# Performance work log

Measured on AMD Instinct MI355X. Metric: run time of the kernel, lower is better.

Reference implementation:

```python
import jax, jax.numpy as jnp
import numpy as np

N_NODES = 50000
EPS = 1e-7      # GENConv message epsilon
BN_EPS = 1e-5   # BatchNorm1d eps
N_AGGR = 2


def setup_inputs() -> dict:
    key = jax.random.key(0)
    ks = jax.random.split(key, 8)
    C = 64
    E = 800000
    x = jax.random.normal(ks[0], (N_NODES, C), dtype=jnp.float32)
    edge_index = jax.random.randint(ks[1], (2, E), 0, N_NODES, dtype=jnp.int64)
    # per-GENConv MLP params, stacked over the N_AGGR layers
    W1 = jax.random.normal(ks[2], (N_AGGR, C, 2 * C), dtype=jnp.float32) * (1.0 / np.sqrt(C))
    b1 = jnp.zeros((N_AGGR, 2 * C), dtype=jnp.float32)
    gamma = jnp.ones((N_AGGR, 2 * C), dtype=jnp.float32)
    beta = jnp.zeros((N_AGGR, 2 * C), dtype=jnp.float32)
    W2 = jax.random.normal(ks[3], (N_AGGR, 2 * C, C), dtype=jnp.float32) * (1.0 / np.sqrt(2 * C))
    b2 = jnp.zeros((N_AGGR, C), dtype=jnp.float32)
    t = jnp.ones((N_AGGR,), dtype=jnp.float32)  # learnable softmax temperature
    return {"x": x, "edge_index": edge_index, "W1": W1, "b1": b1,
            "gamma": gamma, "beta": beta, "W2": W2, "b2": b2, "t": t}


def _gen_conv(x, src, dst, W1_l, b1_l, gamma_l, beta_l, W2_l, b2_l, t_l):
    # message: relu(x_j) + eps  (edge_attr is None)
    m = jax.nn.relu(x[src]) + EPS                      # [E, C]
    # softmax aggregation over edges grouped by destination node
    logits = m * t_l                                   # [E, C]
    seg_max = jax.ops.segment_max(logits, dst, num_segments=N_NODES)  # [N, C]
    ex = jnp.exp(logits - seg_max[dst])                # [E, C]
    den = jax.ops.segment_sum(ex, dst, num_segments=N_NODES)          # [N, C]
    alpha = ex / (den[dst] + 1e-16)                    # [E, C]
    aggr = jax.ops.segment_sum(m * alpha, dst, num_segments=N_NODES)  # [N, C]
    # residual then MLP: Linear(C,2C) -> BatchNorm1d (train-mode stats) -> ReLU -> Linear(2C,C)
    h = aggr + x
    h = h @ W1_l + b1_l                                # [N, 2C]
    mean = h.mean(axis=0)
    var = h.var(axis=0)                                # biased variance (torch BN)
    h = (h - mean) / jnp.sqrt(var + BN_EPS) * gamma_l + beta_l
    h = jax.nn.relu(h)
    h = h @ W2_l + b2_l                                # [N, C]
    return h


def reference(x, edge_index, W1, b1, gamma, beta, W2, b2, t):
    src = edge_index[0]
    dst = edge_index[1]
    for l in range(N_AGGR):
        x = _gen_conv(x, src, dst, W1[l], b1[l], gamma[l], beta[l], W2[l], b2[l], t[l])
        x = jax.nn.relu(x)
        # dropout in eval mode == identity
    return x
```

## Files before the change

kernel.cpp:

```cpp
#include <hip/hip_runtime.h>
#include <math.h>

#define NN 50000
#define EPSM 1e-7f
#define BN_EPS 1e-5f
#define NBK 391


__global__ __launch_bounds__(256) void bucket_hist_kernel(
    const int* __restrict__ dst, int* __restrict__ bhist, int E,
    unsigned* __restrict__ mm0, float* __restrict__ bn0){
  __shared__ int h[NBK];
  int t = threadIdx.x;
  if (blockIdx.x == 0){
    if (t < 64) mm0[t] = 0x7F7FFFFFu;
    else if (t < 128) mm0[t] = 0u;
    bn0[t] = 0.f;
  }
  for (int i = t; i < NBK; i += 256) h[i] = 0;
  __syncthreads();
  int e0 = blockIdx.x * 4096;
  int cnt = min(4096, E - e0);
  for (int i = t; i < cnt; i += 256) atomicAdd(&h[dst[e0 + i] >> 7], 1);
  __syncthreads();
  for (int i = t; i < NBK; i += 256) if (h[i]) atomicAdd(&bhist[i], h[i]);
}

__global__ void bucket_scan_kernel(const int* __restrict__ bhist,
                                   int* __restrict__ bbase, int* __restrict__ gcur){
  int lane = threadIdx.x;
  int loc[7]; int s = 0;
#pragma unroll
  for (int k = 0; k < 7; ++k){
    int i = lane * 7 + k;
    int v = (i < NBK) ? bhist[i] : 0;
    loc[k] = s; s += v;
  }
  int sc = s;
#pragma unroll
  for (int o = 1; o < 64; o <<= 1){
    int n = __shfl_up(sc, o);
    if (lane >= o) sc += n;
  }
  int exc = sc - s;
#pragma unroll
  for (int k = 0; k < 7; ++k){
    int i = lane * 7 + k;
    if (i < NBK){ bbase[i] = exc + loc[k]; gcur[i] = exc + loc[k]; }
    else if (i == NBK) bbase[i] = exc + loc[k];
  }
}

__global__ __launch_bounds__(256) void bucket_scatter_kernel(
    const int* __restrict__ src, const int* __restrict__ dst,
    int* __restrict__ gcur, unsigned* __restrict__ packed_g, int E){
  __shared__ int hist[NBK], offs[NBK], gb[NBK], curk[NBK];
  __shared__ unsigned stage[4096];
  __shared__ int gpos[4096];
  int t = threadIdx.x;
  for (int i = t; i < NBK; i += 256) hist[i] = 0;
  __syncthreads();
  int e0 = blockIdx.x * 4096;
  int cnt = min(4096, E - e0);
  unsigned pk[16]; int bk[16];
  int nmine = 0;
  for (int i = t; i < cnt; i += 256){
    int d = dst[e0 + i], s = src[e0 + i];
    pk[nmine] = ((unsigned)d << 16) | (unsigned)s;
    bk[nmine] = d >> 7;
    atomicAdd(&hist[bk[nmine]], 1);
    ++nmine;
  }
  __syncthreads();
  if (t < 64){
    int loc[7]; int s = 0;
#pragma unroll
    for (int k = 0; k < 7; ++k){
      int i = t * 7 + k;
      int v = (i < NBK) ? hist[i] : 0;
      loc[k] = s; s += v;
    }
    int sc = s;
#pragma unroll
    for (int o = 1; o < 64; o <<= 1){
      int n = __shfl_up(sc, o);
      if (t >= o) sc += n;
    }
    int exc = sc - s;
#pragma unroll
    for (int k = 0; k < 7; ++k){
      int i = t * 7 + k;
      if (i < NBK) offs[i] = exc + loc[k];
    }
  }
  __syncthreads();
  for (int i = t; i < NBK; i += 256){
    int h = hist[i];
    gb[i] = h ? atomicAdd(&gcur[i], h) : 0;
    curk[i] = offs[i];
  }
  __syncthreads();
  for (int k = 0; k < nmine; ++k){
    int b = bk[k];
    int p = atomicAdd(&curk[b], 1);
    stage[p] = pk[k];
    gpos[p] = gb[b] + (p - offs[b]);
  }
  __syncthreads();
  for (int j = t; j < cnt; j += 256) packed_g[gpos[j]] = stage[j];
}

__global__ __launch_bounds__(256) void bucket_place_kernel(
    const unsigned* __restrict__ packed_g, const int* __restrict__ bbase,
    int* __restrict__ start_g, int* __restrict__ end_g,
    unsigned short* __restrict__ srcs_g, int N){
  __shared__ int deg[128], off[128], cur[128];
  __shared__ int sstage[4096];
  int b = blockIdx.x, t = threadIdx.x;
  int beg = bbase[b], cnt = bbase[b + 1] - beg;
  if (t < 128) deg[t] = 0;
  __syncthreads();
  for (int j = t; j < cnt; j += 256)
    atomicAdd(&deg[(packed_g[beg + j] >> 16) & 127], 1);
  __syncthreads();
  if (t < 64){
    int i0 = t * 2;
    int v0 = deg[i0], v1 = deg[i0 + 1];
    int s = v0 + v1;
    int sc = s;
#pragma unroll
    for (int o = 1; o < 64; o <<= 1){
      int n = __shfl_up(sc, o);
      if (t >= o) sc += n;
    }
    int exc = sc - s;
    off[i0] = exc; off[i0 + 1] = exc + v0;
  }
  __syncthreads();
  int node0 = b * 128;
  if (t < 128){
    int node = node0 + t;
    if (node < N){
      start_g[node] = beg + off[t];
      end_g[node] = beg + off[t] + deg[t];
    }
    cur[t] = off[t];
  }
  __syncthreads();
  if (cnt <= 4096){
    for (int j = t; j < cnt; j += 256){
      unsigned p = packed_g[beg + j];
      int lp = atomicAdd(&cur[(p >> 16) & 127], 1);
      sstage[lp] = (int)(p & 0xFFFFu);
    }
    __syncthreads();
    for (int j = t; j < cnt; j += 256)
      srcs_g[beg + j] = (unsigned short)sstage[j];
  } else {
    for (int j = t; j < cnt; j += 256){
      unsigned p = packed_g[beg + j];
      int lp = atomicAdd(&cur[(p >> 16) & 127], 1);
      srcs_g[beg + lp] = (unsigned short)(p & 0xFFFFu);
    }
  }
}


__global__ __launch_bounds__(256) void colminmax_kernel(
    const float* __restrict__ x, unsigned* __restrict__ mm,
    unsigned short* __restrict__ mh, int N){
  __shared__ unsigned smn[256], smx[256];
  int c = threadIdx.x & 63;
  int half = c >> 5, cc = c & 31;
  unsigned short* mhh = mh + (size_t)half * N * 32;
  int slot = blockIdx.x * 4 + (threadIdx.x >> 6);
  float mx = 0.f, mn = 1e30f;
  for (int r = slot; r < N; r += 256 * 4){
    float m = fmaxf(x[r * 64 + c], 0.f) + EPSM;
    unsigned u = __float_as_uint(m);
    u += 0x7FFFu + ((u >> 16) & 1u);
    unsigned short us = (unsigned short)(u >> 16);
    mhh[r * 32 + cc] = us;
    float mb = __uint_as_float(((unsigned)us) << 16);
    mx = fmaxf(mx, mb);
    mn = fminf(mn, mb);
  }
  smn[threadIdx.x] = __float_as_uint(mn);
  smx[threadIdx.x] = __float_as_uint(mx);
  __syncthreads();
  if (threadIdx.x < 64){
    unsigned a = smn[c], b = smn[c + 64], d = smn[c + 128], e = smn[c + 192];
    atomicMin(&mm[c], min(min(a, b), min(d, e)));
    a = smx[c]; b = smx[c + 64]; d = smx[c + 128]; e = smx[c + 192];
    atomicMax(&mm[64 + c], max(max(a, b), max(d, e)));
  }
}


__global__ __launch_bounds__(256) void aggregate_kernel(
    const float* __restrict__ x, const unsigned short* __restrict__ mh,
    const int* __restrict__ start, const int* __restrict__ segend,
    const unsigned short* __restrict__ srcs, const float* __restrict__ tptr,
    int layer, const unsigned* __restrict__ mm, float* __restrict__ h0, int N){
  int node = blockIdx.x * 4 + (threadIdx.x >> 6);
  if (node >= N) return;
  int lane = threadIdx.x & 63;
  int c = lane & 31, slot = lane >> 5;
  int half = blockIdx.y;
  int ch = half * 32 + c;
  const unsigned short* mhh = mh + (size_t)half * N * 32;
  float t = tptr[layer];
  float mn = __uint_as_float(mm[ch]);
  float mx = __uint_as_float(mm[64 + ch]);
  float B = fmaxf(t * mx, t * mn);
  int beg = start[node], end = segend[node];
  float den0 = 0.f, den1 = 0.f, den2 = 0.f, den3 = 0.f;
  float num0 = 0.f, num1 = 0.f, num2 = 0.f, num3 = 0.f;
  int e = beg + slot;
  for (; e + 6 < end; e += 8){
    int s0 = srcs[e], s1 = srcs[e + 2], s2 = srcs[e + 4], s3 = srcs[e + 6];
    float m0 = __uint_as_float(((unsigned)mhh[s0 * 32 + c]) << 16);
    float m1 = __uint_as_float(((unsigned)mhh[s1 * 32 + c]) << 16);
    float m2 = __uint_as_float(((unsigned)mhh[s2 * 32 + c]) << 16);
    float m3 = __uint_as_float(((unsigned)mhh[s3 * 32 + c]) << 16);
    float e0 = __expf(m0 * t - B), e1 = __expf(m1 * t - B);
    float e2 = __expf(m2 * t - B), e3 = __expf(m3 * t - B);
    den0 += e0; num0 += m0 * e0;
    den1 += e1; num1 += m1 * e1;
    den2 += e2; num2 += m2 * e2;
    den3 += e3; num3 += m3 * e3;
  }
  for (; e < end; e += 2){
    int s = srcs[e];
    float m = __uint_as_float(((unsigned)mhh[s * 32 + c]) << 16);
    float ex = __expf(m * t - B);
    den0 += ex; num0 += m * ex;
  }
  float den = (den0 + den1) + (den2 + den3);
  float num = (num0 + num1) + (num2 + num3);
  den += __shfl_xor(den, 32);
  num += __shfl_xor(num, 32);
  if (slot == 0)
    h0[node * 64 + ch] = num / (den + 1e-16f) + x[node * 64 + ch];
}


__global__ __launch_bounds__(256) void gemm1_kernel(
    const float* __restrict__ h0, const float* __restrict__ W1,
    const float* __restrict__ b1, float* __restrict__ h1,
    float* __restrict__ bn, int N,
    unsigned* __restrict__ mm_next, float* __restrict__ bn_next){
  __shared__ float a_lds[64 * 68];
  __shared__ float w_lds[64 * 128];
  int t = threadIdx.x;
  if (mm_next != 0 && blockIdx.x == 0){
    if (t < 64) mm_next[t] = 0x7F7FFFFFu;
    else if (t < 128) mm_next[t] = 0u;
    bn_next[t] = 0.f;
  }
  const float4* wg = (const float4*)W1;
  float4* wl = (float4*)w_lds;
#pragma unroll
  for (int i = 0; i < 8; ++i) wl[t + 256 * i] = wg[t + 256 * i];
  int row0 = blockIdx.x * 64;
#pragma unroll
  for (int i = 0; i < 4; ++i){
    int li = t + 256 * i;
    int r = li >> 4, q = li & 15;
    int gr = row0 + r;
    float4 v = make_float4(0.f, 0.f, 0.f, 0.f);
    if (gr < N) v = ((const float4*)h0)[gr * 16 + q];
    *(float4*)&a_lds[r * 68 + q * 4] = v;
  }
  __syncthreads();
  int tc = t & 31, tr = t >> 5;
  float4 bias = ((const float4*)b1)[tc];
  float acc[8][4];
#pragma unroll
  for (int r = 0; r < 8; ++r){
    acc[r][0] = bias.x; acc[r][1] = bias.y; acc[r][2] = bias.z; acc[r][3] = bias.w;
  }
  for (int k = 0; k < 64; k += 4){
    float4 w0 = *(const float4*)&w_lds[(k + 0) * 128 + tc * 4];
    float4 w1 = *(const float4*)&w_lds[(k + 1) * 128 + tc * 4];
    float4 w2 = *(const float4*)&w_lds[(k + 2) * 128 + tc * 4];
    float4 w3 = *(const float4*)&w_lds[(k + 3) * 128 + tc * 4];
#pragma unroll
    for (int r = 0; r < 8; ++r){
      float4 a = *(const float4*)&a_lds[(tr * 8 + r) * 68 + k];
      acc[r][0] += a.x * w0.x + a.y * w1.x + a.z * w2.x + a.w * w3.x;
      acc[r][1] += a.x * w0.y + a.y * w1.y + a.z * w2.y + a.w * w3.y;
      acc[r][2] += a.x * w0.z + a.y * w1.z + a.z * w2.z + a.w * w3.z;
      acc[r][3] += a.x * w0.w + a.y * w1.w + a.z * w2.w + a.w * w3.w;
    }
  }
  float s[4] = {0.f, 0.f, 0.f, 0.f}, s2[4] = {0.f, 0.f, 0.f, 0.f};
#pragma unroll
  for (int r = 0; r < 8; ++r){
    int gr = row0 + tr * 8 + r;
    if (gr < N){
      *(float4*)&h1[gr * 128 + tc * 4] =
          make_float4(acc[r][0], acc[r][1], acc[r][2], acc[r][3]);
#pragma unroll
      for (int j = 0; j < 4; ++j){ s[j] += acc[r][j]; s2[j] += acc[r][j] * acc[r][j]; }
    }
  }
  __syncthreads();
  float* red = a_lds;
  if (t < 256){ red[t] = 0.f; }
  __syncthreads();
#pragma unroll
  for (int j = 0; j < 4; ++j){
    atomicAdd(&red[tc * 4 + j], s[j]);
    atomicAdd(&red[128 + tc * 4 + j], s2[j]);
  }
  __syncthreads();
  if (t < 256) atomicAdd(&bn[t], red[t]);
}

__global__ __launch_bounds__(256) void gemm2_kernel(
    const float* __restrict__ h1, const float* __restrict__ bn,
    const float* __restrict__ gamma, const float* __restrict__ beta, int layer,
    const float* __restrict__ W2, const float* __restrict__ b2,
    float* __restrict__ xout, int N,
    unsigned* __restrict__ mm_next, unsigned short* __restrict__ mh_next){
  __shared__ float a_lds[64 * 132];
  __shared__ float w_lds[128 * 68];
  __shared__ float ss[256];
  __shared__ unsigned smn[64], smx[64];
  int t = threadIdx.x;
  if (t < 128){
    float mean = bn[t] * (1.f / (float)N);
    float var = bn[128 + t] * (1.f / (float)N) - mean * mean;
    var = fmaxf(var, 0.f);
    float sc = gamma[layer * 128 + t] / sqrtf(var + BN_EPS);
    ss[t] = sc;
    ss[128 + t] = beta[layer * 128 + t] - mean * sc;
  }
  if (t < 64){ smn[t] = 0x7F7FFFFFu; smx[t] = 0u; }
  const float4* wg = (const float4*)W2;
#pragma unroll
  for (int i = 0; i < 8; ++i){
    int li = t + 256 * i;
    int k = li >> 4, q = li & 15;
    *(float4*)&w_lds[k * 68 + q * 4] = wg[li];
  }
  __syncthreads();
  int row0 = blockIdx.x * 64;
#pragma unroll
  for (int i = 0; i < 8; ++i){
    int li = t + 256 * i;
    int r = li >> 5, q = li & 31;
    int gr = row0 + r;
    float4 v = make_float4(0.f, 0.f, 0.f, 0.f);
    if (gr < N) v = ((const float4*)h1)[gr * 32 + q];
    float4 sc = *(const float4*)&ss[q * 4];
    float4 sh = *(const float4*)&ss[128 + q * 4];
    v.x = fmaxf(v.x * sc.x + sh.x, 0.f);
    v.y = fmaxf(v.y * sc.y + sh.y, 0.f);
    v.z = fmaxf(v.z * sc.z + sh.z, 0.f);
    v.w = fmaxf(v.w * sc.w + sh.w, 0.f);
    *(float4*)&a_lds[r * 132 + q * 4] = v;
  }
  __syncthreads();
  int tc = t & 15, tr = t >> 4;
  float4 bias = ((const float4*)b2)[tc];
  float acc[4][4];
#pragma unroll
  for (int r = 0; r < 4; ++r){
    acc[r][0] = bias.x; acc[r][1] = bias.y; acc[r][2] = bias.z; acc[r][3] = bias.w;
  }
  for (int k = 0; k < 128; k += 4){
    float4 w0 = *(const float4*)&w_lds[(k + 0) * 68 + tc * 4];
    float4 w1 = *(const float4*)&w_lds[(k + 1) * 68 + tc * 4];
    float4 w2 = *(const float4*)&w_lds[(k + 2) * 68 + tc * 4];
    float4 w3 = *(const float4*)&w_lds[(k + 3) * 68 + tc * 4];
#pragma unroll
    for (int r = 0; r < 4; ++r){
      float4 a = *(const float4*)&a_lds[(tr * 4 + r) * 132 + k];
      acc[r][0] += a.x * w0.x + a.y * w1.x + a.z * w2.x + a.w * w3.x;
      acc[r][1] += a.x * w0.y + a.y * w1.y + a.z * w2.y + a.w * w3.y;
      acc[r][2] += a.x * w0.z + a.y * w1.z + a.z * w2.z + a.w * w3.z;
      acc[r][3] += a.x * w0.w + a.y * w1.w + a.z * w2.w + a.w * w3.w;
    }
  }
  unsigned mnv[4] = {0x7F7FFFFFu, 0x7F7FFFFFu, 0x7F7FFFFFu, 0x7F7FFFFFu};
  unsigned mxv[4] = {0u, 0u, 0u, 0u};
#pragma unroll
  for (int r = 0; r < 4; ++r){
    int gr = row0 + tr * 4 + r;
    if (gr < N){
      float o0 = fmaxf(acc[r][0], 0.f), o1 = fmaxf(acc[r][1], 0.f);
      float o2 = fmaxf(acc[r][2], 0.f), o3 = fmaxf(acc[r][3], 0.f);
      *(float4*)&xout[gr * 64 + tc * 4] = make_float4(o0, o1, o2, o3);
      if (mh_next != 0){
        unsigned us[4];
        float ov[4] = {o0, o1, o2, o3};
#pragma unroll
        for (int j = 0; j < 4; ++j){
          unsigned u = __float_as_uint(ov[j] + EPSM);
          u += 0x7FFFu + ((u >> 16) & 1u);
          us[j] = u >> 16;
          unsigned fb = us[j] << 16;
          mnv[j] = min(mnv[j], fb);
          mxv[j] = max(mxv[j], fb);
        }
        unsigned short* mh_half = mh_next + (size_t)(tc >> 3) * N * 32;
        ((uint2*)mh_half)[gr * 8 + (tc & 7)] =
            make_uint2(us[0] | (us[1] << 16), us[2] | (us[3] << 16));
      }
    }
  }
  if (mh_next != 0){
    __syncthreads();
#pragma unroll
    for (int j = 0; j < 4; ++j){
      atomicMin(&smn[tc * 4 + j], mnv[j]);
      atomicMax(&smx[tc * 4 + j], mxv[j]);
    }
    __syncthreads();
    if (t < 64){
      atomicMin(&mm_next[t], smn[t]);
      atomicMax(&mm_next[64 + t], smx[t]);
    }
  }
}

extern "C" void kernel_launch(void* const* d_in, const int* in_sizes, int n_in,
                              void* d_out, int out_size, void* d_ws, size_t ws_size,
                              hipStream_t stream) {
  const float* x0    = (const float*)d_in[0];
  const int*   ei    = (const int*)d_in[1];
  const float* W1    = (const float*)d_in[2];
  const float* b1    = (const float*)d_in[3];
  const float* gamma = (const float*)d_in[4];
  const float* beta  = (const float*)d_in[5];
  const float* W2    = (const float*)d_in[6];
  const float* b2    = (const float*)d_in[7];
  const float* tptr  = (const float*)d_in[8];

  const int N = NN;
  const int E = in_sizes[1] / 2;
  const int* src = ei;
  const int* dst = ei + E;

  float* ws  = (float*)d_ws;
  float* h0  = ws;
  float* h1  = h0 + N * 64;
  float* bn0 = h1 + N * 128;
  float* bn1 = bn0 + 256;
  unsigned* mm0 = (unsigned*)(bn1 + 256);
  unsigned* mm1 = mm0 + 128;
  unsigned short* mh = (unsigned short*)(mm1 + 128);
  int* bhist = (int*)(mh + N * 64);
  int* bbase = bhist + NBK;
  int* gcur  = bbase + NBK + 1;
  int* start = gcur + NBK;
  int* segend = start + N;
  unsigned* packed = (unsigned*)(segend + N);
  unsigned short* srcs = (unsigned short*)(packed + E);

  float* out = (float*)d_out;

  const int row_blocks = (N + 63) / 64;
  const int chunk_blocks = (E + 4095) / 4096;
  const dim3 agg_grid((N + 3) / 4, 2);

  hipMemsetAsync(bhist, 0, NBK * sizeof(int), stream);
  bucket_hist_kernel<<<chunk_blocks, 256, 0, stream>>>(dst, bhist, E, mm0, bn0);
  bucket_scan_kernel<<<1, 64, 0, stream>>>(bhist, bbase, gcur);
  bucket_scatter_kernel<<<chunk_blocks, 256, 0, stream>>>(src, dst, gcur, packed, E);
  bucket_place_kernel<<<NBK, 256, 0, stream>>>(packed, bbase, start, segend, srcs, N);

  colminmax_kernel<<<256, 256, 0, stream>>>(x0, mm0, mh, N);
  aggregate_kernel<<<agg_grid, 256, 0, stream>>>(x0, mh, start, segend, srcs,
                                                 tptr, 0, mm0, h0, N);
  gemm1_kernel<<<row_blocks, 256, 0, stream>>>(h0, W1, b1, h1, bn0, N, mm1, bn1);
  gemm2_kernel<<<row_blocks, 256, 0, stream>>>(h1, bn0, gamma, beta, 0, W2, b2,
                                               out, N, mm1, mh);
  aggregate_kernel<<<agg_grid, 256, 0, stream>>>(out, mh, start, segend, srcs,
                                                 tptr, 1, mm1, h0, N);
  gemm1_kernel<<<row_blocks, 256, 0, stream>>>(h0, W1 + 8192, b1 + 128, h1, bn1, N,
                                               (unsigned*)0, (float*)0);
  gemm2_kernel<<<row_blocks, 256, 0, stream>>>(h1, bn1, gamma, beta, 1, W2 + 8192,
                                               b2 + 64, out, N,
                                               (unsigned*)0, (unsigned short*)0);
}
```

Measured before the change: 363.6 us.

## Interleave bf16 message table and process two channels per lane in aggregation

The bf16 message table moves from two channel-half planes to a row-major 64-channel layout. The aggregation kernel now runs in a single grid pass, with each lane loading a 32-bit word that holds two adjacent channels. Each gathered source row becomes one 128-byte access instead of two separate passes over the edge list and index loads. The softmax exponent is rewritten as exp2 with a pre-scaled temperature, at the cost of more registers per thread for the doubled accumulators.

```diff
diff --git a/kernel.cpp b/kernel.cpp
--- a/kernel.cpp
+++ b/kernel.cpp
@@ -5,6 +5,7 @@
 #define EPSM 1e-7f
 #define BN_EPS 1e-5f
 #define NBK 391
+#define LOG2E 1.44269504088896340736f
 
 
 __global__ __launch_bounds__(256) void bucket_hist_kernel(
@@ -171,8 +172,6 @@
     unsigned short* __restrict__ mh, int N){
   __shared__ unsigned smn[256], smx[256];
   int c = threadIdx.x & 63;
-  int half = c >> 5, cc = c & 31;
-  unsigned short* mhh = mh + (size_t)half * N * 32;
   int slot = blockIdx.x * 4 + (threadIdx.x >> 6);
   float mx = 0.f, mn = 1e30f;
   for (int r = slot; r < N; r += 256 * 4){
@@ -180,7 +179,7 @@
     unsigned u = __float_as_uint(m);
     u += 0x7FFFu + ((u >> 16) & 1u);
     unsigned short us = (unsigned short)(u >> 16);
-    mhh[r * 32 + cc] = us;
+    mh[r * 64 + c] = us;
     float mb = __uint_as_float(((unsigned)us) << 16);
     mx = fmaxf(mx, mb);
     mn = fminf(mn, mb);
@@ -198,50 +197,60 @@
 
 
 __global__ __launch_bounds__(256) void aggregate_kernel(
-    const float* __restrict__ x, const unsigned short* __restrict__ mh,
+    const float* __restrict__ x, const unsigned* __restrict__ mh32,
     const int* __restrict__ start, const int* __restrict__ segend,
     const unsigned short* __restrict__ srcs, const float* __restrict__ tptr,
     int layer, const unsigned* __restrict__ mm, float* __restrict__ h0, int N){
   int node = blockIdx.x * 4 + (threadIdx.x >> 6);
   if (node >= N) return;
   int lane = threadIdx.x & 63;
-  int c = lane & 31, slot = lane >> 5;
-  int half = blockIdx.y;
-  int ch = half * 32 + c;
-  const unsigned short* mhh = mh + (size_t)half * N * 32;
-  float t = tptr[layer];
-  float mn = __uint_as_float(mm[ch]);
-  float mx = __uint_as_float(mm[64 + ch]);
-  float B = fmaxf(t * mx, t * mn);
+  int half = lane >> 5, cp = lane & 31;
+  float t2 = tptr[layer] * LOG2E;
+  float mnL = __uint_as_float(mm[2 * cp]);
+  float mxL = __uint_as_float(mm[64 + 2 * cp]);
+  float mnH = __uint_as_float(mm[2 * cp + 1]);
+  float mxH = __uint_as_float(mm[64 + 2 * cp + 1]);
+  float BL = fmaxf(t2 * mxL, t2 * mnL);
+  float BH = fmaxf(t2 * mxH, t2 * mnH);
   int beg = start[node], end = segend[node];
-  float den0 = 0.f, den1 = 0.f, den2 = 0.f, den3 = 0.f;
-  float num0 = 0.f, num1 = 0.f, num2 = 0.f, num3 = 0.f;
-  int e = beg + slot;
+  float dL0=0.f,dL1=0.f,dL2=0.f,dL3=0.f, nL0=0.f,nL1=0.f,nL2=0.f,nL3=0.f;
+  float dH0=0.f,dH1=0.f,dH2=0.f,dH3=0.f, nH0=0.f,nH1=0.f,nH2=0.f,nH3=0.f;
+  int e = beg + half;
   for (; e + 6 < end; e += 8){
     int s0 = srcs[e], s1 = srcs[e + 2], s2 = srcs[e + 4], s3 = srcs[e + 6];
-    float m0 = __uint_as_float(((unsigned)mhh[s0 * 32 + c]) << 16);
-    float m1 = __uint_as_float(((unsigned)mhh[s1 * 32 + c]) << 16);
-    float m2 = __uint_as_float(((unsigned)mhh[s2 * 32 + c]) << 16);
-    float m3 = __uint_as_float(((unsigned)mhh[s3 * 32 + c]) << 16);
-    float e0 = __expf(m0 * t - B), e1 = __expf(m1 * t - B);
-    float e2 = __expf(m2 * t - B), e3 = __expf(m3 * t - B);
-    den0 += e0; num0 += m0 * e0;
-    den1 += e1; num1 += m1 * e1;
-    den2 += e2; num2 += m2 * e2;
-    den3 += e3; num3 += m3 * e3;
+    unsigned u0 = mh32[s0 * 32 + cp], u1 = mh32[s1 * 32 + cp];
+    unsigned u2 = mh32[s2 * 32 + cp], u3 = mh32[s3 * 32 + cp];
+    float mL0 = __uint_as_float(u0 << 16), mH0 = __uint_as_float(u0 & 0xFFFF0000u);
+    float mL1 = __uint_as_float(u1 << 16), mH1 = __uint_as_float(u1 & 0xFFFF0000u);
+    float mL2 = __uint_as_float(u2 << 16), mH2 = __uint_as_float(u2 & 0xFFFF0000u);
+    float mL3 = __uint_as_float(u3 << 16), mH3 = __uint_as_float(u3 & 0xFFFF0000u);
+    float pL0 = exp2f(mL0 * t2 - BL), pH0 = exp2f(mH0 * t2 - BH);
+    float pL1 = exp2f(mL1 * t2 - BL), pH1 = exp2f(mH1 * t2 - BH);
+    float pL2 = exp2f(mL2 * t2 - BL), pH2 = exp2f(mH2 * t2 - BH);
+    float pL3 = exp2f(mL3 * t2 - BL), pH3 = exp2f(mH3 * t2 - BH);
+    dL0 += pL0; nL0 += mL0 * pL0;  dH0 += pH0; nH0 += mH0 * pH0;
+    dL1 += pL1; nL1 += mL1 * pL1;  dH1 += pH1; nH1 += mH1 * pH1;
+    dL2 += pL2; nL2 += mL2 * pL2;  dH2 += pH2; nH2 += mH2 * pH2;
+    dL3 += pL3; nL3 += mL3 * pL3;  dH3 += pH3; nH3 += mH3 * pH3;
   }
   for (; e < end; e += 2){
     int s = srcs[e];
-    float m = __uint_as_float(((unsigned)mhh[s * 32 + c]) << 16);
-    float ex = __expf(m * t - B);
-    den0 += ex; num0 += m * ex;
-  }
-  float den = (den0 + den1) + (den2 + den3);
-  float num = (num0 + num1) + (num2 + num3);
-  den += __shfl_xor(den, 32);
-  num += __shfl_xor(num, 32);
-  if (slot == 0)
-    h0[node * 64 + ch] = num / (den + 1e-16f) + x[node * 64 + ch];
+    unsigned u = mh32[s * 32 + cp];
+    float mL = __uint_as_float(u << 16), mH = __uint_as_float(u & 0xFFFF0000u);
+    float pL = exp2f(mL * t2 - BL), pH = exp2f(mH * t2 - BH);
+    dL0 += pL; nL0 += mL * pL;  dH0 += pH; nH0 += mH * pH;
+  }
+  float dL = (dL0 + dL1) + (dL2 + dL3), nL = (nL0 + nL1) + (nL2 + nL3);
+  float dH = (dH0 + dH1) + (dH2 + dH3), nH = (nH0 + nH1) + (nH2 + nH3);
+  dL += __shfl_xor(dL, 32); nL += __shfl_xor(nL, 32);
+  dH += __shfl_xor(dH, 32); nH += __shfl_xor(nH, 32);
+  if (half == 0){
+    float2 xv = ((const float2*)x)[node * 32 + cp];
+    float2 o;
+    o.x = nL / (dL + 1e-16f) + xv.x;
+    o.y = nH / (dH + 1e-16f) + xv.y;
+    ((float2*)h0)[node * 32 + cp] = o;
+  }
 }
 
 
@@ -405,8 +414,7 @@
           mnv[j] = min(mnv[j], fb);
           mxv[j] = max(mxv[j], fb);
         }
-        unsigned short* mh_half = mh_next + (size_t)(tc >> 3) * N * 32;
-        ((uint2*)mh_half)[gr * 8 + (tc & 7)] =
+        ((uint2*)mh_next)[gr * 16 + tc] =
             make_uint2(us[0] | (us[1] << 16), us[2] | (us[3] << 16));
       }
     }
@@ -464,7 +472,7 @@
 
   const int row_blocks = (N + 63) / 64;
   const int chunk_blocks = (E + 4095) / 4096;
-  const dim3 agg_grid((N + 3) / 4, 2);
+  const int agg_blocks = (N + 3) / 4;
 
   hipMemsetAsync(bhist, 0, NBK * sizeof(int), stream);
   bucket_hist_kernel<<<chunk_blocks, 256, 0, stream>>>(dst, bhist, E, mm0, bn0);
@@ -473,13 +481,13 @@
   bucket_place_kernel<<<NBK, 256, 0, stream>>>(packed, bbase, start, segend, srcs, N);
 
   colminmax_kernel<<<256, 256, 0, stream>>>(x0, mm0, mh, N);
-  aggregate_kernel<<<agg_grid, 256, 0, stream>>>(x0, mh, start, segend, srcs,
-                                                 tptr, 0, mm0, h0, N);
+  aggregate_kernel<<<agg_blocks, 256, 0, stream>>>(x0, (const unsigned*)mh, start,
+                                                   segend, srcs, tptr, 0, mm0, h0, N);
   gemm1_kernel<<<row_blocks, 256, 0, stream>>>(h0, W1, b1, h1, bn0, N, mm1, bn1);
   gemm2_kernel<<<row_blocks, 256, 0, stream>>>(h1, bn0, gamma, beta, 0, W2, b2,
                                                out, N, mm1, mh);
-  aggregate_kernel<<<agg_grid, 256, 0, stream>>>(out, mh, start, segend, srcs,
-                                                 tptr, 1, mm1, h0, N);
+  aggregate_kernel<<<agg_blocks, 256, 0, stream>>>(out, (const unsigned*)mh, start,
+                                                   segend, srcs, tptr, 1, mm1, h0, N);
   gemm1_kernel<<<row_blocks, 256, 0, stream>>>(h0, W1 + 8192, b1 + 128, h1, bn1, N,
                                                (unsigned*)0, (float*)0);
   gemm2_kernel<<<row_blocks, 256, 0, stream>>>(h1, bn1, gamma, beta, 1, W2 + 8192,
```

Result: faster. 335.4 us (-7.8%).
